# Kernel optimization log

Measured on AMD Instinct MI355X. Metric: run time of the kernel, lower is better.

The kernel has to match this reference:

```python
import jax, jax.numpy as jnp
import numpy as np

B, LV, LQ, VDIM, HID, NHEADS = 32, 1000, 1200, 128, 512, 8
HEAD_DIM = HID // NHEADS
PER = 0.2
BN_EPS = 1e-5
SCALE = float(np.sqrt(HEAD_DIM))


def _pos_enc(x):
    # x: [B, L, D]; sinusoidal PE as in PositionalEncoding (max_len slice == direct compute)
    L, D = x.shape[1], x.shape[2]
    pos = jnp.arange(L, dtype=x.dtype)[:, None]                      # [L,1]
    div = jnp.exp(jnp.arange(0, D, 2, dtype=x.dtype) * (-np.log(10000.0) / D))
    ang = pos * div                                                  # [L, D/2]
    pe = jnp.stack([jnp.sin(ang), jnp.cos(ang)], axis=-1).reshape(L, D)  # interleave sin/cos
    return x + pe[None]


def _heads(x):
    # [B, L, HID] -> [B, H, L, d]
    b, l, _ = x.shape
    return x.reshape(b, l, NHEADS, HEAD_DIM).transpose(0, 2, 1, 3)


def setup_inputs() -> dict:
    key = jax.random.key(0)
    ks = jax.random.split(key, 12)
    s = 1.0 / np.sqrt(VDIM)
    inp = {
        "query": jax.random.normal(ks[0], (B, LV, VDIM), jnp.float32),
        "key": jax.random.normal(ks[1], (B, LQ, VDIM), jnp.float32),
        "att": jax.random.normal(ks[2], (B, 4, LV), jnp.float32),
        "Wq": jax.random.uniform(ks[3], (VDIM, HID), jnp.float32, -s, s),
        "bq": jnp.zeros((HID,), jnp.float32),
        "Wk": jax.random.uniform(ks[4], (VDIM, HID), jnp.float32, -s, s),
        "bk": jnp.zeros((HID,), jnp.float32),
        "Wv1": jax.random.uniform(ks[5], (VDIM, HID), jnp.float32, -s, s),
        "bv1": jnp.zeros((HID,), jnp.float32),
        "Wv2": jax.random.uniform(ks[6], (VDIM, HID), jnp.float32, -s, s),
        "bv2": jnp.zeros((HID,), jnp.float32),
        "bn_gamma": jnp.ones((HID,), jnp.float32),
        "bn_beta": jnp.zeros((HID,), jnp.float32),
        "bn_mean": jnp.zeros((HID,), jnp.float32),
        "bn_var": jnp.ones((HID,), jnp.float32),
    }
    return inp


def reference(query, key, att, Wq, bq, Wk, bk, Wv1, bv1, Wv2, bv2,
              bn_gamma, bn_beta, bn_mean, bn_var):
    len_pro = int(PER * att.shape[-1])                       # 200, static
    scores = att.max(axis=1)                                 # [B, LV]
    idx = jnp.argsort(-scores, axis=1)[:, :len_pro]          # top-k token indices, descending
    q_sel = jnp.take_along_axis(query, idx[:, :, None], axis=1)  # [B, len_pro, VDIM]

    # projections (dropout = identity in eval); PosEncV applied to both query and key
    Q = _heads(_pos_enc(q_sel) @ Wq + bq)                    # [B,H,Lv',d]
    K = _heads(_pos_enc(key) @ Wk + bk)                      # [B,H,Lq,d]
    V1 = _heads(q_sel @ Wv1 + bv1)                           # [B,H,Lv',d]
    V2 = _heads(key @ Wv2 + bv2)                             # [B,H,Lq,d]

    attn = jnp.einsum('bhvd,bhqd->bhvq', Q, K) / SCALE       # [B,H,Lv',Lq] (softmax=False)

    # trilinear pooling: einsum('bhvk,bhvq,bhqk->bhk', V1, attn, V2)
    t = jnp.einsum('bhvq,bhqk->bhvk', attn, V2)              # [B,H,Lv',d]
    x = jnp.sum(V1 * t, axis=2)                              # [B,H,d]
    x = x.reshape(x.shape[0], HID)

    # BatchNorm1d (eval mode, running stats)
    x = (x - bn_mean) / jnp.sqrt(bn_var + BN_EPS) * bn_gamma + bn_beta

    attn_avg = attn.sum(axis=1) / NHEADS                     # [B,Lv',Lq]
    return x, idx, attn_avg
```

## Files before the change

kernel.cpp:

```cpp
#include <hip/hip_runtime.h>
#include <hip/hip_bf16.h>

#define NB 32
#define LV 1000
#define LQ 1200
#define VD 128
#define HID 512
#define NH 8
#define HD 64
#define LP 200
#define LQP 1216
#define LPP 256
#define GM 4
#define GN 2

typedef __attribute__((ext_vector_type(8))) short s8v;
typedef __attribute__((ext_vector_type(4))) float f4v;

union FragU { s8v v; unsigned short u[8]; };

__device__ __forceinline__ unsigned short f2bf(float f) {
    __hip_bfloat16 h = __float2bfloat16(f);
    return *reinterpret_cast<unsigned short*>(&h);
}

__global__ __launch_bounds__(256) void topk_kernel(const float* __restrict__ att,
                                                   int* __restrict__ idx_ws,
                                                   float* __restrict__ out_idx) {
    __shared__ float s[1024];
    __shared__ int   si[1024];
    int b = blockIdx.x, tid = threadIdx.x;
    for (int i = tid; i < 1024; i += 256) {
        float v = -INFINITY;
        if (i < LV) {
            const float* p = att + (size_t)b * 4 * LV + i;
            v = fmaxf(fmaxf(p[0], p[LV]), fmaxf(p[2 * LV], p[3 * LV]));
        }
        s[i] = v; si[i] = i;
    }
    __syncthreads();
    for (int k = 2; k <= 1024; k <<= 1) {
        for (int j = k >> 1; j > 0; j >>= 1) {
            for (int i = tid; i < 1024; i += 256) {
                int l = i ^ j;
                if (l > i) {
                    float a = s[i], c = s[l];
                    int ia = si[i], ic = si[l];
                    bool aFirst = (a > c) || (a == c && ia < ic);
                    bool desc = ((i & k) == 0);
                    if (desc != aFirst) { s[i] = c; s[l] = a; si[i] = ic; si[l] = ia; }
                }
            }
            __syncthreads();
        }
    }
    for (int i = tid; i < LP; i += 256) {
        int v = si[i];
        idx_ws[b * LP + i]  = v;
        out_idx[b * LP + i] = (float)v;
    }
}

__global__ __launch_bounds__(256) void prep_kernel(
    float* __restrict__ pe,
    const float* __restrict__ w0, const float* __restrict__ w1,
    const float* __restrict__ w2, const float* __restrict__ w3,
    unsigned short* __restrict__ t0, unsigned short* __restrict__ t1,
    unsigned short* __restrict__ t2, unsigned short* __restrict__ t3)
{
    __shared__ unsigned short Ts[64][72];
    int bx = blockIdx.x, tid = threadIdx.x;
    if (bx < 600) {
        int t = bx * 256 + tid;
        if (t < LQ * VD) {
            int r = t >> 7, c = t & 127;
            int i = c >> 1;
            float div = expf((float)(2 * i) * -0.07195578415606394f);
            float ang = (float)r * div;
            pe[t] = (c & 1) ? cosf(ang) : sinf(ang);
        }
        return;
    }
    int idx = bx - 600;
    int mat = idx >> 4, rem = idx & 15;
    int k0 = (rem & 1) * 64, n0 = (rem >> 1) * 64;
    const float* W; unsigned short* T;
    switch (mat) {
        case 0:  W = w0; T = t0; break;
        case 1:  W = w1; T = t1; break;
        case 2:  W = w2; T = t2; break;
        default: W = w3; T = t3; break;
    }
    #pragma unroll
    for (int e = 0; e < 2; ++e) {
        int flat = tid + e * 256;
        int kk = flat >> 3, n8 = (flat & 7) * 8;
        const float* p = W + (size_t)(k0 + kk) * HID + n0 + n8;
        float4 f0 = *(const float4*)p, f1 = *(const float4*)(p + 4);
        Ts[n8 + 0][kk] = f2bf(f0.x); Ts[n8 + 1][kk] = f2bf(f0.y);
        Ts[n8 + 2][kk] = f2bf(f0.z); Ts[n8 + 3][kk] = f2bf(f0.w);
        Ts[n8 + 4][kk] = f2bf(f1.x); Ts[n8 + 5][kk] = f2bf(f1.y);
        Ts[n8 + 6][kk] = f2bf(f1.z); Ts[n8 + 7][kk] = f2bf(f1.w);
    }
    __syncthreads();
    #pragma unroll
    for (int e = 0; e < 2; ++e) {
        int flat = tid + e * 256;
        int nn = flat >> 3, k8 = (flat & 7) * 8;
        uint4 pk;
        pk.x = (unsigned)Ts[nn][k8 + 0] | ((unsigned)Ts[nn][k8 + 1] << 16);
        pk.y = (unsigned)Ts[nn][k8 + 2] | ((unsigned)Ts[nn][k8 + 3] << 16);
        pk.z = (unsigned)Ts[nn][k8 + 4] | ((unsigned)Ts[nn][k8 + 5] << 16);
        pk.w = (unsigned)Ts[nn][k8 + 6] | ((unsigned)Ts[nn][k8 + 7] << 16);
        *(uint4*)&T[(size_t)(n0 + nn) * VD + k0 + k8] = pk;
    }
}

__global__ __launch_bounds__(256) void proj_kernel(
    const float* __restrict__ query, const float* __restrict__ key,
    const int* __restrict__ idxws, const float* __restrict__ pe,
    const unsigned short* __restrict__ Wqt, const unsigned short* __restrict__ Wkt,
    const unsigned short* __restrict__ Wv1t, const unsigned short* __restrict__ Wv2t,
    const float* __restrict__ bq, const float* __restrict__ bk,
    const float* __restrict__ bv1, const float* __restrict__ bv2,
    unsigned short* __restrict__ Qp, unsigned short* __restrict__ Kp,
    unsigned short* __restrict__ Qt, unsigned short* __restrict__ Kt,
    unsigned short* __restrict__ V1t, unsigned short* __restrict__ V2t)
{
    __shared__ unsigned short Tls[4][64][72];
    int z = blockIdx.z;
    int p = z >> 5, b = z & 31;
    bool gath = (p >= 2);
    if (gath && blockIdx.x >= 2) return;

    const float* src = gath ? query : key;
    int srcRows = gath ? LV : LQ;
    int rows    = gath ? LP : LQ;
    int Lpad    = gath ? LPP : LQP;
    bool usePE  = (p == 0) || (p == 2);
    const unsigned short* Wt = (p == 0) ? Wkt : (p == 1) ? Wv2t : (p == 2) ? Wqt : Wv1t;
    const float* bias        = (p == 0) ? bk  : (p == 1) ? bv2  : (p == 2) ? bq  : bv1;
    unsigned short* dst  = (p == 0) ? Kp : (p == 2) ? Qp : nullptr;
    unsigned short* dstT = (p == 0) ? Kt : (p == 1) ? V2t : (p == 2) ? Qt : V1t;

    int lane = threadIdx.x & 63, w = threadIdx.x >> 6;
    int rbase = blockIdx.x * 128 + (w >> 1) * 64;
    int nbase = blockIdx.y * 128 + (w & 1) * 64;
    if (rbase >= Lpad) return;
    int lc = lane & 15, lg = lane >> 4;

    int srow[4], prow[4];
    #pragma unroll
    for (int i = 0; i < 4; ++i) {
        int rc = min(rbase + i * 16 + lc, rows - 1);
        prow[i] = rc;
        srow[i] = gath ? idxws[b * LP + rc] : rc;
    }

    f4v acc[4][4] = {};
    for (int kk = 0; kk < VD; kk += 32) {
        s8v af[4], bfr[4];
        #pragma unroll
        for (int i = 0; i < 4; ++i) {
            const float* pp = src + ((size_t)b * srcRows + srow[i]) * VD + kk + lg * 8;
            float4 f0 = *(const float4*)pp, f1 = *(const float4*)(pp + 4);
            float fv[8] = {f0.x, f0.y, f0.z, f0.w, f1.x, f1.y, f1.z, f1.w};
            if (usePE) {
                const float* q = pe + (size_t)prow[i] * VD + kk + lg * 8;
                float4 p0 = *(const float4*)q, p1 = *(const float4*)(q + 4);
                float pv[8] = {p0.x, p0.y, p0.z, p0.w, p1.x, p1.y, p1.z, p1.w};
                #pragma unroll
                for (int e = 0; e < 8; ++e) fv[e] += pv[e];
            }
            FragU fu;
            #pragma unroll
            for (int e = 0; e < 8; ++e) fu.u[e] = f2bf(fv[e]);
            af[i] = fu.v;
        }
        #pragma unroll
        for (int j = 0; j < 4; ++j)
            bfr[j] = *(const s8v*)&Wt[(size_t)(nbase + j * 16 + lc) * VD + kk + lg * 8];
        #pragma unroll
        for (int i = 0; i < 4; ++i)
            #pragma unroll
            for (int j = 0; j < 4; ++j)
                acc[i][j] = __builtin_amdgcn_mfma_f32_16x16x32_bf16(af[i], bfr[j], acc[i][j], 0, 0, 0);
    }

    float bb[4];
    #pragma unroll
    for (int j = 0; j < 4; ++j) bb[j] = bias[nbase + j * 16 + lc];

    unsigned short* Tw = &Tls[w][0][0];

    if (dst) {
        #pragma unroll
        for (int i = 0; i < 4; ++i)
            #pragma unroll
            for (int j = 0; j < 4; ++j)
                #pragma unroll
                for (int reg = 0; reg < 4; ++reg)
                    Tw[(i * 16 + lg * 4 + reg) * 72 + j * 16 + lc] =
                        f2bf(acc[i][j][reg] + bb[j]);
        #pragma unroll
        for (int e = 0; e < 8; ++e) {
            int c = lane + e * 64;
            int rr = c >> 3, cc = (c & 7) * 8;
            s8v vv = *(const s8v*)&Tw[rr * 72 + cc];
            int gr = rbase + rr;
            if (gr < rows)
                *(s8v*)&dst[((size_t)b * rows + gr) * HID + nbase + cc] = vv;
        }
    }
    #pragma unroll
    for (int i = 0; i < 4; ++i)
        #pragma unroll
        for (int j = 0; j < 4; ++j)
            #pragma unroll
            for (int reg = 0; reg < 4; ++reg) {
                int r = rbase + i * 16 + lg * 4 + reg;
                Tw[(j * 16 + lc) * 72 + i * 16 + lg * 4 + reg] =
                    (r < rows) ? f2bf(acc[i][j][reg] + bb[j]) : (unsigned short)0;
            }
    #pragma unroll
    for (int e = 0; e < 8; ++e) {
        int c = lane + e * 64;
        int nn = c >> 3, cc = (c & 7) * 8;
        s8v vv = *(const s8v*)&Tw[nn * 72 + cc];
        *(s8v*)&dstT[((size_t)b * HID + nbase + nn) * Lpad + rbase + cc] = vv;
    }
}

__global__ __launch_bounds__(256) void attnavg_kernel(
    const unsigned short* __restrict__ Qp, const unsigned short* __restrict__ Kp,
    float* __restrict__ outA)
{
    __shared__ float Tf[4][32][68];
    int b = blockIdx.z;
    int lane = threadIdx.x & 63, w = threadIdx.x >> 6;
    int vbase = blockIdx.y * 128 + (w >> 1) * 64;
    int qbase = blockIdx.x * 128 + (w & 1) * 64;
    if (qbase >= LQ || vbase >= LP) return;
    int lc = lane & 15, lg = lane >> 4;

    int vr[4], qr[4];
    #pragma unroll
    for (int i = 0; i < 4; ++i) vr[i] = min(vbase + i * 16 + lc, LP - 1);
    #pragma unroll
    for (int j = 0; j < 4; ++j) qr[j] = min(qbase + j * 16 + lc, LQ - 1);

    f4v acc[4][4] = {};
    for (int kk = 0; kk < HID; kk += 32) {
        s8v af[4], bfr[4];
        #pragma unroll
        for (int i = 0; i < 4; ++i)
            af[i] = *(const s8v*)&Qp[((size_t)b * LP + vr[i]) * HID + kk + lg * 8];
        #pragma unroll
        for (int j = 0; j < 4; ++j)
            bfr[j] = *(const s8v*)&Kp[((size_t)b * LQ + qr[j]) * HID + kk + lg * 8];
        #pragma unroll
        for (int i = 0; i < 4; ++i)
            #pragma unroll
            for (int j = 0; j < 4; ++j)
                acc[i][j] = __builtin_amdgcn_mfma_f32_16x16x32_bf16(af[i], bfr[j], acc[i][j], 0, 0, 0);
    }

    float* Tw = &Tf[w][0][0];
    #pragma unroll
    for (int round = 0; round < 2; ++round) {
        #pragma unroll
        for (int ii = 0; ii < 2; ++ii) {
            int i = round * 2 + ii;
            #pragma unroll
            for (int j = 0; j < 4; ++j)
                #pragma unroll
                for (int reg = 0; reg < 4; ++reg)
                    Tw[(ii * 16 + lg * 4 + reg) * 68 + j * 16 + lc] =
                        acc[i][j][reg] * 0.015625f;
        }
        #pragma unroll
        for (int e = 0; e < 8; ++e) {
            int c = lane + e * 64;
            int rr = c >> 4, cc = (c & 15) * 4;
            float4 vv = *(const float4*)&Tw[rr * 68 + cc];
            int gv = vbase + round * 32 + rr;
            int gq = qbase + cc;
            if (gv < LP && gq < LQ)
                *(float4*)&outA[((size_t)b * LP + gv) * LQ + gq] = vv;
        }
    }
}

__global__ __launch_bounds__(64) void pair_kernel(
    const unsigned short* __restrict__ Kt, const unsigned short* __restrict__ V2t,
    const unsigned short* __restrict__ Qt, const unsigned short* __restrict__ V1t,
    float* __restrict__ Mp, float* __restrict__ Np)
{
    int g = blockIdx.x;
    const unsigned short *At, *Bt; float* outP;
    int LPAD, NCH, G, slab;
    if (g < GM) { At = Kt; Bt = V2t; outP = Mp; LPAD = LQP; NCH = 38; G = GM; slab = g; }
    else        { At = Qt; Bt = V1t; outP = Np; LPAD = LPP; NCH = 8;  G = GN; slab = g - GM; }
    int bh = blockIdx.y, b = bh >> 3, h = bh & 7;
    int lane = threadIdx.x, lc = lane & 15, lg = lane >> 4;
    const unsigned short* Ah = At + ((size_t)b * HID + h * HD) * LPAD;
    const unsigned short* Bh = Bt + ((size_t)b * HID + h * HD) * LPAD;
    f4v acc[4][4] = {};
    for (int c = slab; c < NCH; c += G) {
        int r0 = c * 32 + lg * 8;
        s8v af[4], bfr[4];
        #pragma unroll
        for (int i = 0; i < 4; ++i)
            af[i] = *(const s8v*)&Ah[(size_t)(i * 16 + lc) * LPAD + r0];
        #pragma unroll
        for (int j = 0; j < 4; ++j)
            bfr[j] = *(const s8v*)&Bh[(size_t)(j * 16 + lc) * LPAD + r0];
        #pragma unroll
        for (int i = 0; i < 4; ++i)
            #pragma unroll
            for (int j = 0; j < 4; ++j)
                acc[i][j] = __builtin_amdgcn_mfma_f32_16x16x32_bf16(af[i], bfr[j], acc[i][j], 0, 0, 0);
    }
    float* op = outP + ((size_t)slab * 256 + bh) * 4096;
    #pragma unroll
    for (int i = 0; i < 4; ++i)
        #pragma unroll
        for (int reg = 0; reg < 4; ++reg) {
            int d = i * 16 + lg * 4 + reg;
            #pragma unroll
            for (int j = 0; j < 4; ++j)
                op[d * 64 + j * 16 + lc] = acc[i][j][reg];
        }
}

__global__ __launch_bounds__(256) void xout_kernel(
    const float* __restrict__ Mp, const float* __restrict__ Np,
    const float* __restrict__ gamma, const float* __restrict__ beta,
    const float* __restrict__ mean, const float* __restrict__ var,
    float* __restrict__ outX)
{
    int bh = blockIdx.x, b = bh >> 3, h = bh & 7;
    int tid = threadIdx.x;
    int k = tid & 63, dg = tid >> 6;
    float s = 0.f;
    for (int d = dg * 16; d < dg * 16 + 16; ++d) {
        int o = d * 64 + k;
        float m = 0.f, n = 0.f;
        #pragma unroll
        for (int g = 0; g < GM; ++g) m += Mp[((size_t)g * 256 + bh) * 4096 + o];
        #pragma unroll
        for (int g = 0; g < GN; ++g) n += Np[((size_t)g * 256 + bh) * 4096 + o];
        s += m * n;
    }
    __shared__ float red[4][64];
    red[dg][k] = s;
    __syncthreads();
    if (tid < 64) {
        float x = (red[0][tid] + red[1][tid] + red[2][tid] + red[3][tid]) * 0.125f;
        int c = h * HD + tid;
        outX[(size_t)b * HID + c] =
            (x - mean[c]) * rsqrtf(var[c] + 1e-5f) * gamma[c] + beta[c];
    }
}

extern "C" void kernel_launch(void* const* d_in, const int* in_sizes, int n_in,
                              void* d_out, int out_size, void* d_ws, size_t ws_size,
                              hipStream_t stream) {
    const float* query = (const float*)d_in[0];
    const float* key   = (const float*)d_in[1];
    const float* att   = (const float*)d_in[2];
    const float* Wq  = (const float*)d_in[3];
    const float* bq  = (const float*)d_in[4];
    const float* Wk  = (const float*)d_in[5];
    const float* bk  = (const float*)d_in[6];
    const float* Wv1 = (const float*)d_in[7];
    const float* bv1 = (const float*)d_in[8];
    const float* Wv2 = (const float*)d_in[9];
    const float* bv2 = (const float*)d_in[10];
    const float* gamma = (const float*)d_in[11];
    const float* beta  = (const float*)d_in[12];
    const float* mean  = (const float*)d_in[13];
    const float* var   = (const float*)d_in[14];

    float* out    = (float*)d_out;
    float* outX   = out;
    float* outIdx = out + 16384;
    float* outA   = out + 22784;

    char* ws = (char*)d_ws;
    size_t off = 0;
    auto carve = [&](size_t bytes) {
        void* p = ws + off; off += (bytes + 255) & ~(size_t)255; return p;
    };
    int*            idxws = (int*)carve((size_t)NB * LP * 4);
    unsigned short* Wqt   = (unsigned short*)carve((size_t)HID * VD * 2);
    unsigned short* Wkt   = (unsigned short*)carve((size_t)HID * VD * 2);
    unsigned short* Wv1t  = (unsigned short*)carve((size_t)HID * VD * 2);
    unsigned short* Wv2t  = (unsigned short*)carve((size_t)HID * VD * 2);
    unsigned short* Kp    = (unsigned short*)carve((size_t)NB * LQ * HID * 2);
    unsigned short* Qt    = (unsigned short*)carve((size_t)NB * HID * LPP * 2);
    unsigned short* Kt    = (unsigned short*)carve((size_t)NB * HID * LQP * 2);
    unsigned short* V1t   = (unsigned short*)carve((size_t)NB * HID * LPP * 2);
    unsigned short* V2t   = (unsigned short*)carve((size_t)NB * HID * LQP * 2);
    float*          pe    = (float*)carve((size_t)LQ * VD * 4);
    unsigned short* Qp    = (unsigned short*)carve((size_t)NB * LP * HID * 2);
    float* Mp = (float*)Kp;
    float* Np = (float*)((char*)Kp + (size_t)GM * 256 * 4096 * 4);
    (void)ws_size; (void)in_sizes; (void)n_in; (void)out_size;

    topk_kernel<<<dim3(NB), dim3(256), 0, stream>>>(att, idxws, outIdx);
    prep_kernel<<<dim3(664), dim3(256), 0, stream>>>(
        pe, Wq, Wk, Wv1, Wv2, Wqt, Wkt, Wv1t, Wv2t);

    proj_kernel<<<dim3(10, 4, 128), dim3(256), 0, stream>>>(
        query, key, idxws, pe, Wqt, Wkt, Wv1t, Wv2t, bq, bk, bv1, bv2,
        Qp, Kp, Qt, Kt, V1t, V2t);

    attnavg_kernel<<<dim3(10, 2, NB), dim3(256), 0, stream>>>(Qp, Kp, outA);

    pair_kernel<<<dim3(GM + GN, 256), dim3(64), 0, stream>>>(
        Kt, V2t, Qt, V1t, Mp, Np);

    xout_kernel<<<dim3(256), dim3(256), 0, stream>>>(
        Mp, Np, gamma, beta, mean, var, outX);
}
```

Before: 338.2 us.

## Precompute positional-encoding projection and drop LDS transposes in projection and attention epilogues

The positional-encoding contribution (PE @ W + bias) is computed once per weight in a new kernel, so the per-batch projection only multiplies the raw inputs and adds the stored PE projection in its epilogue. The projection kernel is split into separate blocks for transposed and row-major outputs, and swapped MFMA operand order lets results be written directly as vector stores instead of going through LDS transposes. The attention-average and pair kernels use the same operand swap to avoid LDS staging. The top-k sort now uses 1024 threads per block. This adds an extra kernel, extra workspace, and recomputes the K and Q GEMMs in two block types, and adding PE after the bf16 GEMM changes rounding slightly.

```diff
diff --git a/kernel.cpp b/kernel.cpp
--- a/kernel.cpp
+++ b/kernel.cpp
@@ -24,40 +24,38 @@
     return *reinterpret_cast<unsigned short*>(&h);
 }
 
-__global__ __launch_bounds__(256) void topk_kernel(const float* __restrict__ att,
-                                                   int* __restrict__ idx_ws,
-                                                   float* __restrict__ out_idx) {
+__global__ __launch_bounds__(1024) void topk_kernel(const float* __restrict__ att,
+                                                    int* __restrict__ idx_ws,
+                                                    float* __restrict__ out_idx) {
     __shared__ float s[1024];
     __shared__ int   si[1024];
     int b = blockIdx.x, tid = threadIdx.x;
-    for (int i = tid; i < 1024; i += 256) {
+    {
         float v = -INFINITY;
-        if (i < LV) {
-            const float* p = att + (size_t)b * 4 * LV + i;
+        if (tid < LV) {
+            const float* p = att + (size_t)b * 4 * LV + tid;
             v = fmaxf(fmaxf(p[0], p[LV]), fmaxf(p[2 * LV], p[3 * LV]));
         }
-        s[i] = v; si[i] = i;
+        s[tid] = v; si[tid] = tid;
     }
     __syncthreads();
     for (int k = 2; k <= 1024; k <<= 1) {
         for (int j = k >> 1; j > 0; j >>= 1) {
-            for (int i = tid; i < 1024; i += 256) {
-                int l = i ^ j;
-                if (l > i) {
-                    float a = s[i], c = s[l];
-                    int ia = si[i], ic = si[l];
-                    bool aFirst = (a > c) || (a == c && ia < ic);
-                    bool desc = ((i & k) == 0);
-                    if (desc != aFirst) { s[i] = c; s[l] = a; si[i] = ic; si[l] = ia; }
-                }
+            int i = tid, l = i ^ j;
+            if (l > i) {
+                float a = s[i], c = s[l];
+                int ia = si[i], ic = si[l];
+                bool aFirst = (a > c) || (a == c && ia < ic);
+                bool desc = ((i & k) == 0);
+                if (desc != aFirst) { s[i] = c; s[l] = a; si[i] = ic; si[l] = ia; }
             }
             __syncthreads();
         }
     }
-    for (int i = tid; i < LP; i += 256) {
-        int v = si[i];
-        idx_ws[b * LP + i]  = v;
-        out_idx[b * LP + i] = (float)v;
+    if (tid < LP) {
+        int v = si[tid];
+        idx_ws[b * LP + tid]  = v;
+        out_idx[b * LP + tid] = (float)v;
     }
 }
 
@@ -116,118 +114,209 @@
     }
 }
 
+__global__ __launch_bounds__(256) void pew_kernel(
+    const float* __restrict__ pe,
+    const unsigned short* __restrict__ Wkt, const unsigned short* __restrict__ Wqt,
+    const float* __restrict__ bk, const float* __restrict__ bq,
+    float* __restrict__ PEWk, float* __restrict__ PEWkT,
+    float* __restrict__ PEWq, float* __restrict__ PEWqT)
+{
+    int x = blockIdx.x, yb = blockIdx.y;
+    bool kMat = (x < 10);
+    int rows = kMat ? LQ : LP;
+    int Lpad = kMat ? LQP : LPP;
+    const unsigned short* Wt = kMat ? Wkt : Wqt;
+    const float* bias = kMat ? bk : bq;
+    float* PW  = kMat ? PEWk : PEWq;
+    float* PWT = kMat ? PEWkT : PEWqT;
+    int xb = kMat ? x : x - 10;
+    int lane = threadIdx.x & 63, w = threadIdx.x >> 6;
+    int rbase = xb * 128 + (w >> 1) * 64;
+    int nbase = yb * 128 + (w & 1) * 64;
+    if (rbase >= Lpad) return;
+    int lc = lane & 15, lg = lane >> 4;
+
+    int prow[4];
+    #pragma unroll
+    for (int i = 0; i < 4; ++i) prow[i] = min(rbase + i * 16 + lc, rows - 1);
+
+    f4v acc[4][4] = {};
+    for (int kk = 0; kk < VD; kk += 32) {
+        s8v af[4], bfr[4];
+        #pragma unroll
+        for (int i = 0; i < 4; ++i) {
+            const float* pp = pe + (size_t)prow[i] * VD + kk + lg * 8;
+            float4 f0 = *(const float4*)pp, f1 = *(const float4*)(pp + 4);
+            FragU fu;
+            fu.u[0]=f2bf(f0.x); fu.u[1]=f2bf(f0.y); fu.u[2]=f2bf(f0.z); fu.u[3]=f2bf(f0.w);
+            fu.u[4]=f2bf(f1.x); fu.u[5]=f2bf(f1.y); fu.u[6]=f2bf(f1.z); fu.u[7]=f2bf(f1.w);
+            af[i] = fu.v;
+        }
+        #pragma unroll
+        for (int j = 0; j < 4; ++j)
+            bfr[j] = *(const s8v*)&Wt[(size_t)(nbase + j * 16 + lc) * VD + kk + lg * 8];
+        #pragma unroll
+        for (int i = 0; i < 4; ++i)
+            #pragma unroll
+            for (int j = 0; j < 4; ++j)
+                acc[i][j] = __builtin_amdgcn_mfma_f32_16x16x32_bf16(bfr[j], af[i], acc[i][j], 0, 0, 0);
+    }
+    #pragma unroll
+    for (int i = 0; i < 4; ++i) {
+        int r = rbase + i * 16 + lc;
+        #pragma unroll
+        for (int j = 0; j < 4; ++j) {
+            int n0 = nbase + j * 16 + lg * 4;
+            float4 b4 = *(const float4*)&bias[n0];
+            float4 v = {acc[i][j][0] + b4.x, acc[i][j][1] + b4.y,
+                        acc[i][j][2] + b4.z, acc[i][j][3] + b4.w};
+            *(float4*)&PW[(size_t)r * HID + n0] = v;
+            PWT[(size_t)(n0 + 0) * Lpad + r] = v.x;
+            PWT[(size_t)(n0 + 1) * Lpad + r] = v.y;
+            PWT[(size_t)(n0 + 2) * Lpad + r] = v.z;
+            PWT[(size_t)(n0 + 3) * Lpad + r] = v.w;
+        }
+    }
+}
+
 __global__ __launch_bounds__(256) void proj_kernel(
     const float* __restrict__ query, const float* __restrict__ key,
-    const int* __restrict__ idxws, const float* __restrict__ pe,
+    const int* __restrict__ idxws,
     const unsigned short* __restrict__ Wqt, const unsigned short* __restrict__ Wkt,
     const unsigned short* __restrict__ Wv1t, const unsigned short* __restrict__ Wv2t,
-    const float* __restrict__ bq, const float* __restrict__ bk,
     const float* __restrict__ bv1, const float* __restrict__ bv2,
+    const float* __restrict__ PEWk, const float* __restrict__ PEWkT,
+    const float* __restrict__ PEWq, const float* __restrict__ PEWqT,
     unsigned short* __restrict__ Qp, unsigned short* __restrict__ Kp,
     unsigned short* __restrict__ Qt, unsigned short* __restrict__ Kt,
     unsigned short* __restrict__ V1t, unsigned short* __restrict__ V2t)
 {
-    __shared__ unsigned short Tls[4][64][72];
-    int z = blockIdx.z;
-    int p = z >> 5, b = z & 31;
+    int id = blockIdx.x, b = blockIdx.z;
+    bool Rp = (id >= 96);
+    int p, xb;
+    if (!Rp) {
+        if (id < 40)      { p = 0; xb = id >> 2; }
+        else if (id < 80) { p = 1; xb = (id - 40) >> 2; }
+        else if (id < 88) { p = 2; xb = (id - 80) >> 2; }
+        else              { p = 3; xb = (id - 88) >> 2; }
+    } else {
+        int t = id - 96;
+        if (t < 40) { p = 0; xb = t >> 2; }
+        else        { p = 2; xb = (t - 40) >> 2; }
+    }
+    int yb = id & 3;
     bool gath = (p >= 2);
-    if (gath && blockIdx.x >= 2) return;
-
     const float* src = gath ? query : key;
     int srcRows = gath ? LV : LQ;
-    int rows    = gath ? LP : LQ;
-    int Lpad    = gath ? LPP : LQP;
-    bool usePE  = (p == 0) || (p == 2);
+    int rows = gath ? LP : LQ;
+    int Lpad = gath ? LPP : LQP;
     const unsigned short* Wt = (p == 0) ? Wkt : (p == 1) ? Wv2t : (p == 2) ? Wqt : Wv1t;
-    const float* bias        = (p == 0) ? bk  : (p == 1) ? bv2  : (p == 2) ? bq  : bv1;
-    unsigned short* dst  = (p == 0) ? Kp : (p == 2) ? Qp : nullptr;
-    unsigned short* dstT = (p == 0) ? Kt : (p == 1) ? V2t : (p == 2) ? Qt : V1t;
 
     int lane = threadIdx.x & 63, w = threadIdx.x >> 6;
-    int rbase = blockIdx.x * 128 + (w >> 1) * 64;
-    int nbase = blockIdx.y * 128 + (w & 1) * 64;
+    int rbase = xb * 128 + (w >> 1) * 64;
+    int nbase = yb * 128 + (w & 1) * 64;
     if (rbase >= Lpad) return;
     int lc = lane & 15, lg = lane >> 4;
 
-    int srow[4], prow[4];
+    int srow[4];
     #pragma unroll
     for (int i = 0; i < 4; ++i) {
         int rc = min(rbase + i * 16 + lc, rows - 1);
-        prow[i] = rc;
         srow[i] = gath ? idxws[b * LP + rc] : rc;
     }
 
-    f4v acc[4][4] = {};
-    for (int kk = 0; kk < VD; kk += 32) {
-        s8v af[4], bfr[4];
+    if (!Rp) {
+        unsigned short* dstT = (p == 0) ? Kt : (p == 1) ? V2t : (p == 2) ? Qt : V1t;
+        const float* PWT  = (p == 0) ? PEWkT : (p == 2) ? PEWqT : nullptr;
+        const float* bias = (p == 1) ? bv2 : bv1;
+        bool usePE = (p == 0) || (p == 2);
+        f4v acc[4][4] = {};
+        for (int kk = 0; kk < VD; kk += 32) {
+            s8v af[4], bfr[4];
+            #pragma unroll
+            for (int i = 0; i < 4; ++i) {
+                const float* pp = src + ((size_t)b * srcRows + srow[i]) * VD + kk + lg * 8;
+                float4 f0 = *(const float4*)pp, f1 = *(const float4*)(pp + 4);
+                FragU fu;
+                fu.u[0]=f2bf(f0.x); fu.u[1]=f2bf(f0.y); fu.u[2]=f2bf(f0.z); fu.u[3]=f2bf(f0.w);
+                fu.u[4]=f2bf(f1.x); fu.u[5]=f2bf(f1.y); fu.u[6]=f2bf(f1.z); fu.u[7]=f2bf(f1.w);
+                af[i] = fu.v;
+            }
+            #pragma unroll
+            for (int j = 0; j < 4; ++j)
+                bfr[j] = *(const s8v*)&Wt[(size_t)(nbase + j * 16 + lc) * VD + kk + lg * 8];
+            #pragma unroll
+            for (int i = 0; i < 4; ++i)
+                #pragma unroll
+                for (int j = 0; j < 4; ++j)
+                    acc[i][j] = __builtin_amdgcn_mfma_f32_16x16x32_bf16(af[i], bfr[j], acc[i][j], 0, 0, 0);
+        }
+        float bbc[4];
+        #pragma unroll
+        for (int j = 0; j < 4; ++j) bbc[j] = usePE ? 0.f : bias[nbase + j * 16 + lc];
         #pragma unroll
         for (int i = 0; i < 4; ++i) {
-            const float* pp = src + ((size_t)b * srcRows + srow[i]) * VD + kk + lg * 8;
-            float4 f0 = *(const float4*)pp, f1 = *(const float4*)(pp + 4);
-            float fv[8] = {f0.x, f0.y, f0.z, f0.w, f1.x, f1.y, f1.z, f1.w};
-            if (usePE) {
-                const float* q = pe + (size_t)prow[i] * VD + kk + lg * 8;
-                float4 p0 = *(const float4*)q, p1 = *(const float4*)(q + 4);
-                float pv[8] = {p0.x, p0.y, p0.z, p0.w, p1.x, p1.y, p1.z, p1.w};
+            int rb = rbase + i * 16 + lg * 4;
+            #pragma unroll
+            for (int j = 0; j < 4; ++j) {
+                int n = nbase + j * 16 + lc;
+                float a0, a1, a2, a3;
+                if (usePE) {
+                    float4 t4 = *(const float4*)&PWT[(size_t)n * Lpad + rb];
+                    a0 = t4.x; a1 = t4.y; a2 = t4.z; a3 = t4.w;
+                } else { a0 = a1 = a2 = a3 = bbc[j]; }
+                unsigned short h0 = (rb + 0 < rows) ? f2bf(acc[i][j][0] + a0) : (unsigned short)0;
+                unsigned short h1 = (rb + 1 < rows) ? f2bf(acc[i][j][1] + a1) : (unsigned short)0;
+                unsigned short h2 = (rb + 2 < rows) ? f2bf(acc[i][j][2] + a2) : (unsigned short)0;
+                unsigned short h3 = (rb + 3 < rows) ? f2bf(acc[i][j][3] + a3) : (unsigned short)0;
+                uint2 pk;
+                pk.x = (unsigned)h0 | ((unsigned)h1 << 16);
+                pk.y = (unsigned)h2 | ((unsigned)h3 << 16);
+                *(uint2*)&dstT[((size_t)b * HID + n) * Lpad + rb] = pk;
+            }
+        }
+    } else {
+        unsigned short* dst = (p == 0) ? Kp : Qp;
+        const float* PW = (p == 0) ? PEWk : PEWq;
+        f4v acc[4][4] = {};
+        for (int kk = 0; kk < VD; kk += 32) {
+            s8v af[4], bfr[4];
+            #pragma unroll
+            for (int i = 0; i < 4; ++i) {
+                const float* pp = src + ((size_t)b * srcRows + srow[i]) * VD + kk + lg * 8;
+                float4 f0 = *(const float4*)pp, f1 = *(const float4*)(pp + 4);
+                FragU fu;
+                fu.u[0]=f2bf(f0.x); fu.u[1]=f2bf(f0.y); fu.u[2]=f2bf(f0.z); fu.u[3]=f2bf(f0.w);
+                fu.u[4]=f2bf(f1.x); fu.u[5]=f2bf(f1.y); fu.u[6]=f2bf(f1.z); fu.u[7]=f2bf(f1.w);
+                af[i] = fu.v;
+            }
+            #pragma unroll
+            for (int j = 0; j < 4; ++j)
+                bfr[j] = *(const s8v*)&Wt[(size_t)(nbase + j * 16 + lc) * VD + kk + lg * 8];
+            #pragma unroll
+            for (int i = 0; i < 4; ++i)
                 #pragma unroll
-                for (int e = 0; e < 8; ++e) fv[e] += pv[e];
+                for (int j = 0; j < 4; ++j)
+                    acc[i][j] = __builtin_amdgcn_mfma_f32_16x16x32_bf16(bfr[j], af[i], acc[i][j], 0, 0, 0);
+        }
+        #pragma unroll
+        for (int i = 0; i < 4; ++i) {
+            int r = rbase + i * 16 + lc;
+            if (r >= rows) continue;
+            const float* pw = PW + (size_t)r * HID;
+            unsigned short* dr = dst + ((size_t)b * rows + r) * HID;
+            #pragma unroll
+            for (int j = 0; j < 4; ++j) {
+                int n0 = nbase + j * 16 + lg * 4;
+                float4 a4 = *(const float4*)&pw[n0];
+                uint2 pk;
+                pk.x = (unsigned)f2bf(acc[i][j][0] + a4.x) |
+                       ((unsigned)f2bf(acc[i][j][1] + a4.y) << 16);
+                pk.y = (unsigned)f2bf(acc[i][j][2] + a4.z) |
+                       ((unsigned)f2bf(acc[i][j][3] + a4.w) << 16);
+                *(uint2*)&dr[n0] = pk;
             }
-            FragU fu;
-            #pragma unroll
-            for (int e = 0; e < 8; ++e) fu.u[e] = f2bf(fv[e]);
-            af[i] = fu.v;
-        }
-        #pragma unroll
-        for (int j = 0; j < 4; ++j)
-            bfr[j] = *(const s8v*)&Wt[(size_t)(nbase + j * 16 + lc) * VD + kk + lg * 8];
-        #pragma unroll
-        for (int i = 0; i < 4; ++i)
-            #pragma unroll
-            for (int j = 0; j < 4; ++j)
-                acc[i][j] = __builtin_amdgcn_mfma_f32_16x16x32_bf16(af[i], bfr[j], acc[i][j], 0, 0, 0);
-    }
-
-    float bb[4];
-    #pragma unroll
-    for (int j = 0; j < 4; ++j) bb[j] = bias[nbase + j * 16 + lc];
-
-    unsigned short* Tw = &Tls[w][0][0];
-
-    if (dst) {
-        #pragma unroll
-        for (int i = 0; i < 4; ++i)
-            #pragma unroll
-            for (int j = 0; j < 4; ++j)
-                #pragma unroll
-                for (int reg = 0; reg < 4; ++reg)
-                    Tw[(i * 16 + lg * 4 + reg) * 72 + j * 16 + lc] =
-                        f2bf(acc[i][j][reg] + bb[j]);
-        #pragma unroll
-        for (int e = 0; e < 8; ++e) {
-            int c = lane + e * 64;
-            int rr = c >> 3, cc = (c & 7) * 8;
-            s8v vv = *(const s8v*)&Tw[rr * 72 + cc];
-            int gr = rbase + rr;
-            if (gr < rows)
-                *(s8v*)&dst[((size_t)b * rows + gr) * HID + nbase + cc] = vv;
-        }
-    }
-    #pragma unroll
-    for (int i = 0; i < 4; ++i)
-        #pragma unroll
-        for (int j = 0; j < 4; ++j)
-            #pragma unroll
-            for (int reg = 0; reg < 4; ++reg) {
-                int r = rbase + i * 16 + lg * 4 + reg;
-                Tw[(j * 16 + lc) * 72 + i * 16 + lg * 4 + reg] =
-                    (r < rows) ? f2bf(acc[i][j][reg] + bb[j]) : (unsigned short)0;
-            }
-    #pragma unroll
-    for (int e = 0; e < 8; ++e) {
-        int c = lane + e * 64;
-        int nn = c >> 3, cc = (c & 7) * 8;
-        s8v vv = *(const s8v*)&Tw[nn * 72 + cc];
-        *(s8v*)&dstT[((size_t)b * HID + nbase + nn) * Lpad + rbase + cc] = vv;
+        }
     }
 }
 
@@ -235,7 +324,6 @@
     const unsigned short* __restrict__ Qp, const unsigned short* __restrict__ Kp,
     float* __restrict__ outA)
 {
-    __shared__ float Tf[4][32][68];
     int b = blockIdx.z;
     int lane = threadIdx.x & 63, w = threadIdx.x >> 6;
     int vbase = blockIdx.y * 128 + (w >> 1) * 64;
@@ -243,50 +331,40 @@
     if (qbase >= LQ || vbase >= LP) return;
     int lc = lane & 15, lg = lane >> 4;
 
-    int vr[4], qr[4];
-    #pragma unroll
-    for (int i = 0; i < 4; ++i) vr[i] = min(vbase + i * 16 + lc, LP - 1);
-    #pragma unroll
-    for (int j = 0; j < 4; ++j) qr[j] = min(qbase + j * 16 + lc, LQ - 1);
+    int qr[4], vr[4];
+    #pragma unroll
+    for (int i = 0; i < 4; ++i) qr[i] = min(qbase + i * 16 + lc, LQ - 1);
+    #pragma unroll
+    for (int j = 0; j < 4; ++j) vr[j] = min(vbase + j * 16 + lc, LP - 1);
 
     f4v acc[4][4] = {};
     for (int kk = 0; kk < HID; kk += 32) {
         s8v af[4], bfr[4];
         #pragma unroll
         for (int i = 0; i < 4; ++i)
-            af[i] = *(const s8v*)&Qp[((size_t)b * LP + vr[i]) * HID + kk + lg * 8];
+            af[i] = *(const s8v*)&Kp[((size_t)b * LQ + qr[i]) * HID + kk + lg * 8];
         #pragma unroll
         for (int j = 0; j < 4; ++j)
-            bfr[j] = *(const s8v*)&Kp[((size_t)b * LQ + qr[j]) * HID + kk + lg * 8];
+            bfr[j] = *(const s8v*)&Qp[((size_t)b * LP + vr[j]) * HID + kk + lg * 8];
         #pragma unroll
         for (int i = 0; i < 4; ++i)
             #pragma unroll
             for (int j = 0; j < 4; ++j)
                 acc[i][j] = __builtin_amdgcn_mfma_f32_16x16x32_bf16(af[i], bfr[j], acc[i][j], 0, 0, 0);
     }
-
-    float* Tw = &Tf[w][0][0];
-    #pragma unroll
-    for (int round = 0; round < 2; ++round) {
-        #pragma unroll
-        for (int ii = 0; ii < 2; ++ii) {
-            int i = round * 2 + ii;
-            #pragma unroll
-            for (int j = 0; j < 4; ++j)
-                #pragma unroll
-                for (int reg = 0; reg < 4; ++reg)
-                    Tw[(ii * 16 + lg * 4 + reg) * 68 + j * 16 + lc] =
-                        acc[i][j][reg] * 0.015625f;
-        }
-        #pragma unroll
-        for (int e = 0; e < 8; ++e) {
-            int c = lane + e * 64;
-            int rr = c >> 4, cc = (c & 15) * 4;
-            float4 vv = *(const float4*)&Tw[rr * 68 + cc];
-            int gv = vbase + round * 32 + rr;
-            int gq = qbase + cc;
-            if (gv < LP && gq < LQ)
-                *(float4*)&outA[((size_t)b * LP + gv) * LQ + gq] = vv;
+    const float sc = 1.0f / 64.0f;
+    #pragma unroll
+    for (int j = 0; j < 4; ++j) {
+        int v = vbase + j * 16 + lc;
+        if (v >= LP) continue;
+        float* base = outA + ((size_t)b * LP + v) * LQ;
+        #pragma unroll
+        for (int i = 0; i < 4; ++i) {
+            int q0 = qbase + i * 16 + lg * 4;
+            if (q0 + 3 >= LQ) continue;
+            float4 o = {acc[i][j][0] * sc, acc[i][j][1] * sc,
+                        acc[i][j][2] * sc, acc[i][j][3] * sc};
+            *(float4*)&base[q0] = o;
         }
     }
 }
@@ -319,18 +397,19 @@
         for (int i = 0; i < 4; ++i)
             #pragma unroll
             for (int j = 0; j < 4; ++j)
-                acc[i][j] = __builtin_amdgcn_mfma_f32_16x16x32_bf16(af[i], bfr[j], acc[i][j], 0, 0, 0);
+                acc[i][j] = __builtin_amdgcn_mfma_f32_16x16x32_bf16(bfr[j], af[i], acc[i][j], 0, 0, 0);
     }
     float* op = outP + ((size_t)slab * 256 + bh) * 4096;
     #pragma unroll
-    for (int i = 0; i < 4; ++i)
-        #pragma unroll
-        for (int reg = 0; reg < 4; ++reg) {
-            int d = i * 16 + lg * 4 + reg;
-            #pragma unroll
-            for (int j = 0; j < 4; ++j)
-                op[d * 64 + j * 16 + lc] = acc[i][j][reg];
-        }
+    for (int i = 0; i < 4; ++i) {
+        int d = i * 16 + lc;
+        #pragma unroll
+        for (int j = 0; j < 4; ++j) {
+            int k0 = j * 16 + lg * 4;
+            float4 o = {acc[i][j][0], acc[i][j][1], acc[i][j][2], acc[i][j][3]};
+            *(float4*)&op[d * 64 + k0] = o;
+        }
+    }
 }
 
 __global__ __launch_bounds__(256) void xout_kernel(
@@ -404,17 +483,23 @@
     unsigned short* V2t   = (unsigned short*)carve((size_t)NB * HID * LQP * 2);
     float*          pe    = (float*)carve((size_t)LQ * VD * 4);
     unsigned short* Qp    = (unsigned short*)carve((size_t)NB * LP * HID * 2);
+    float*          PEWk  = (float*)carve((size_t)LQP * HID * 4);
+    float*          PEWkT = (float*)carve((size_t)HID * LQP * 4);
+    float*          PEWq  = (float*)carve((size_t)LPP * HID * 4);
+    float*          PEWqT = (float*)carve((size_t)HID * LPP * 4);
     float* Mp = (float*)Kp;
     float* Np = (float*)((char*)Kp + (size_t)GM * 256 * 4096 * 4);
     (void)ws_size; (void)in_sizes; (void)n_in; (void)out_size;
 
-    topk_kernel<<<dim3(NB), dim3(256), 0, stream>>>(att, idxws, outIdx);
+    topk_kernel<<<dim3(NB), dim3(1024), 0, stream>>>(att, idxws, outIdx);
     prep_kernel<<<dim3(664), dim3(256), 0, stream>>>(
         pe, Wq, Wk, Wv1, Wv2, Wqt, Wkt, Wv1t, Wv2t);
-
-    proj_kernel<<<dim3(10, 4, 128), dim3(256), 0, stream>>>(
-        query, key, idxws, pe, Wqt, Wkt, Wv1t, Wv2t, bq, bk, bv1, bv2,
-        Qp, Kp, Qt, Kt, V1t, V2t);
+    pew_kernel<<<dim3(12, 4), dim3(256), 0, stream>>>(
+        pe, Wkt, Wqt, bk, bq, PEWk, PEWkT, PEWq, PEWqT);
+
+    proj_kernel<<<dim3(144, 1, NB), dim3(256), 0, stream>>>(
+        query, key, idxws, Wqt, Wkt, Wv1t, Wv2t, bv1, bv2,
+        PEWk, PEWkT, PEWq, PEWqT, Qp, Kp, Qt, Kt, V1t, V2t);
 
     attnavg_kernel<<<dim3(10, 2, NB), dim3(256), 0, stream>>>(Qp, Kp, outA);
 
```

After: 382.9 us. 13.2% more time.
